# Performance work log

Hardware: AMD Instinct MI355X
Metric: run time of the kernel (lower is better)

Reference implementation:

```python
import jax, jax.numpy as jnp
import numpy as np

N, E, B, D, H, L = 50000, 800000, 16, 64, 128, 2


def _lin(h, w, b):
    return h @ w + b


def _scatter_mean(v, idx, n):
    s = jax.ops.segment_sum(v, idx, num_segments=n)
    c = jax.ops.segment_sum(jnp.ones((v.shape[0],), v.dtype), idx, num_segments=n)
    return s / jnp.maximum(c, 1.0)[:, None]


def setup_inputs() -> dict:
    key = jax.random.key(0)
    ks = iter(jax.random.split(key, 40))

    def p(*shape):
        return jax.random.normal(next(ks), shape, dtype=jnp.float32) * 0.05

    inp = {
        "x": jax.random.normal(next(ks), (N, D), dtype=jnp.float32),
        "edge_attr": jax.random.normal(next(ks), (E, D), dtype=jnp.float32),
        "u": jax.random.normal(next(ks), (B, D), dtype=jnp.float32),
        "e_w1": p(L, 4 * D, H), "e_b1": p(L, H),
        "e_w2": p(L, H, H), "e_b2": p(L, H),
        "e_w3": p(L, H, D), "e_b3": p(L, D),
        "n1_w1": p(L, 2 * D, H), "n1_b1": p(L, H),
        "n1_w2": p(L, H, H), "n1_b2": p(L, H),
        "n2_w1": p(L, D + H + D, H), "n2_b1": p(L, H),
        "n2_w2": p(L, H, D), "n2_b2": p(L, D),
        "g_w1": p(L, 3 * D, H), "g_b1": p(L, H),
        "g_w2": p(L, H, D), "g_b2": p(L, D),
        "edge_index": jax.random.randint(next(ks), (2, E), 0, N, dtype=jnp.int32),
        "batch": jnp.sort(jax.random.randint(next(ks), (N,), 0, B, dtype=jnp.int32)),
    }
    return inp


def _forward(x, edge_attr, u, params, edge_index, batch):
    row, col = edge_index[0], edge_index[1]
    eb = batch[row]  # [E] graph id per edge
    x0, e0, u0 = x, edge_attr, u
    for l in range(L):
        (e_w1, e_b1, e_w2, e_b2, e_w3, e_b3,
         n1_w1, n1_b1, n1_w2, n1_b2,
         n2_w1, n2_b1, n2_w2, n2_b2,
         g_w1, g_b1, g_w2, g_b2) = [pm[l] for pm in params]
        # Edge model: [E, e+2n+u] -> MLP -> [E, D]
        h = jnp.concatenate([x[row], x[col], edge_attr, u[eb]], axis=1)
        h = jax.nn.relu(_lin(h, e_w1, e_b1))
        h = jax.nn.relu(_lin(h, e_w2, e_b2))
        edge_attr = _lin(h, e_w3, e_b3)
        # Node model: gather src node + edge, MLP1, scatter_mean onto dest, MLP2
        se = jnp.concatenate([x[row], edge_attr], axis=1)  # [E, 2D]
        se = _lin(jax.nn.relu(_lin(se, n1_w1, n1_b1)), n1_w2, n1_b2)
        agg = _scatter_mean(se, col, N)  # [N, H]
        xh = jnp.concatenate([x, agg, u[batch]], axis=1)
        x = _lin(jax.nn.relu(_lin(xh, n2_w1, n2_b1)), n2_w2, n2_b2)
        # Global model: per-graph means of updated nodes/edges
        e_agg = _scatter_mean(edge_attr, eb, B)
        n_agg = _scatter_mean(x, batch, B)
        uh = jnp.concatenate([u, n_agg, e_agg], axis=1)
        u = _lin(jax.nn.relu(_lin(uh, g_w1, g_b1)), g_w2, g_b2)
    return x + x0, edge_attr + e0, u + u0


def reference(x, edge_attr, u, e_w1, e_b1, e_w2, e_b2, e_w3, e_b3, n1_w1, n1_b1, n1_w2, n1_b2, n2_w1, n2_b1, n2_w2, n2_b2, g_w1, g_b1, g_w2, g_b2, edge_index, batch):
    params = (e_w1, e_b1, e_w2, e_b2, e_w3, e_b3,
              n1_w1, n1_b1, n1_w2, n1_b2,
              n2_w1, n2_b1, n2_w2, n2_b2,
              g_w1, g_b1, g_w2, g_b2)
    return _forward(x, edge_attr, u, params, edge_index, batch)
```

## Files before the change

### kernel.cpp

```cpp
#include <hip/hip_runtime.h>

#define N_NODES 50000
#define E_EDGES 800000
#define NG 16
#define DD 64
#define HH 128
#define NB_SCAN 49

typedef __attribute__((ext_vector_type(8))) __bf16 bf16x8;
typedef __attribute__((ext_vector_type(4))) float f32x4;
typedef unsigned int uint;
typedef unsigned short ushort;
typedef __attribute__((ext_vector_type(4))) uint uint4v;

#define MFMA16(a,b,c) __builtin_amdgcn_mfma_f32_16x16x32_bf16((a),(b),(c),0,0,0)

__device__ __forceinline__ ushort f2bf(float f){
  uint u = __builtin_bit_cast(uint, f);
  u += 0x7fffu + ((u >> 16) & 1u);
  return (ushort)(u >> 16);
}
__device__ __forceinline__ uint pk2(float a, float b){
  return (uint)f2bf(a) | ((uint)f2bf(b) << 16);
}
__device__ __forceinline__ float bflo(uint u){ return __builtin_bit_cast(float, u << 16); }
__device__ __forceinline__ float bfhi(uint u){ return __builtin_bit_cast(float, u & 0xffff0000u); }

__device__ __forceinline__ bf16x8 ldfrag(const char* base, int row, int byteoff){
  uint4v v = *(const uint4v*)(base + row*256 + (byteoff ^ ((row & 7) << 4)));
  return __builtin_bit_cast(bf16x8, v);
}
__device__ __forceinline__ uint4v ld_chunk(const char* base, int row, int c16){
  return *(const uint4v*)(base + row*256 + ((c16*16) ^ ((row & 7) << 4)));
}
__device__ __forceinline__ void st_h(char* base, int row, int col, float v){
  *(ushort*)(base + row*256 + ((col*2) ^ ((row & 7) << 4))) = f2bf(v);
}
__device__ __forceinline__ void st_chunk(char* base, int row, int c16, uint4v v){
  *(uint4v*)(base + row*256 + ((c16*16) ^ ((row & 7) << 4))) = v;
}
__device__ __forceinline__ void pack16(char* dst, int r, int c16, const float* src){
  float4 lo = *(const float4*)src;
  float4 hi = *(const float4*)(src + 4);
  uint4v v; v.x = pk2(lo.x, lo.y); v.y = pk2(lo.z, lo.w);
  v.z = pk2(hi.x, hi.y); v.w = pk2(hi.z, hi.w);
  st_chunk(dst, r, c16, v);
}

__device__ __forceinline__ void stage_b(char* sB, const ushort* wt,
                                        int Nout, int Ktot, int koff, int t, int stride){
  for (int task = t; task < Nout*16; task += stride){
    int n = task >> 4, c = task & 15;
    uint4v v = *(const uint4v*)(wt + (long)n*Ktot + koff + c*8);
    st_chunk(sB, n, c, v);
  }
}

__device__ __forceinline__ void gemmN4(const char* A, const char* B,
                                       int mw, int nh, int l15, int lhi, f32x4* acc){
  #pragma unroll
  for (int kt = 0; kt < 4; ++kt){
    bf16x8 a = ldfrag(A, mw*16 + l15, kt*64 + lhi*16);
    #pragma unroll
    for (int n = 0; n < 4; ++n){
      bf16x8 bb = ldfrag(B, (nh*4 + n)*16 + l15, kt*64 + lhi*16);
      acc[n] = MFMA16(a, bb, acc[n]);
    }
  }
}
template<bool RELU>
__device__ __forceinline__ void epiN4(char* dst, const f32x4* acc, const float* bias,
                                      int mw, int nh, int l15, int lhi){
  #pragma unroll
  for (int n = 0; n < 4; ++n){
    int col = nh*64 + n*16 + l15;
    float bv = bias[col];
    #pragma unroll
    for (int j = 0; j < 4; ++j){
      int r = mw*16 + lhi*4 + j;
      float v = acc[n][j] + bv;
      if (RELU) v = fmaxf(v, 0.f);
      st_h(dst, r, col, v);
    }
  }
}

template<int NT>
__device__ __forceinline__ void gemm_acc(const char* A, const char* B,
                                         int wv, int l15, int lhi, f32x4* acc){
  #pragma unroll
  for (int kt = 0; kt < 4; ++kt){
    bf16x8 a = ldfrag(A, wv*16 + l15, kt*64 + lhi*16);
    #pragma unroll
    for (int n = 0; n < NT; ++n){
      bf16x8 bb = ldfrag(B, n*16 + l15, kt*64 + lhi*16);
      acc[n] = MFMA16(a, bb, acc[n]);
    }
  }
}
template<int NT, bool RELU>
__device__ __forceinline__ void epi_lds(char* dst, const f32x4* acc, const float* bias,
                                        int wv, int l15, int lhi){
  #pragma unroll
  for (int n = 0; n < NT; ++n){
    float bv = bias[n*16 + l15];
    #pragma unroll
    for (int j = 0; j < 4; ++j){
      int r = wv*16 + lhi*4 + j;
      float v = acc[n][j] + bv;
      if (RELU) v = fmaxf(v, 0.f);
      st_h(dst, r, n*16 + l15, v);
    }
  }
}

__global__ void pack_weights(const float* __restrict__ e1, const float* __restrict__ e2,
                             const float* __restrict__ e3, const float* __restrict__ n11,
                             const float* __restrict__ n12, const float* __restrict__ n21,
                             const float* __restrict__ n22, ushort* __restrict__ out){
  int idx = blockIdx.x * 256 + threadIdx.x;
  int l = idx / 131072, r = idx % 131072;
  const float* src; int K, N, off;
  if      (r <  32768){ src = e1;  K = 256; N = 128; off = 0; }
  else if (r <  49152){ src = e2;  K = 128; N = 128; off = 32768; }
  else if (r <  57344){ src = e3;  K = 128; N = 64;  off = 49152; }
  else if (r <  73728){ src = n11; K = 128; N = 128; off = 57344; }
  else if (r <  90112){ src = n12; K = 128; N = 128; off = 73728; }
  else if (r < 122880){ src = n21; K = 256; N = 128; off = 90112; }
  else                { src = n22; K = 128; N = 64;  off = 122880; }
  int q = r - off; int k = q / N; int n = q % N;
  out[(long)l*131072 + off + n*K + k] = f2bf(src[(long)l*K*N + q]);
}

__global__ void hist_kernel(const int* __restrict__ edge_index, const int* __restrict__ batch,
                            int* __restrict__ deg, float* __restrict__ cnt_eb){
  __shared__ float h[NG];
  int t = threadIdx.x;
  if (t < NG) h[t] = 0.f;
  __syncthreads();
  int e = blockIdx.x * 256 + t;
  if (e < E_EDGES){
    atomicAdd(deg + edge_index[E_EDGES + e], 1);
    atomicAdd(&h[batch[edge_index[e]]], 1.f);
  }
  __syncthreads();
  if (t < NG) atomicAdd(cnt_eb + t, h[t]);
}
__global__ void count_nodes_kernel(const int* __restrict__ batch, float* __restrict__ cnt_b){
  __shared__ float h[NG];
  int t = threadIdx.x;
  if (t < NG) h[t] = 0.f;
  __syncthreads();
  int n = blockIdx.x * 256 + t;
  if (n < N_NODES) atomicAdd(&h[batch[n]], 1.f);
  __syncthreads();
  if (t < NG) atomicAdd(cnt_b + t, h[t]);
}
__global__ void scan_a(const int* __restrict__ deg, int* __restrict__ bsum){
  __shared__ int red[1024];
  int i = blockIdx.x*1024 + threadIdx.x;
  red[threadIdx.x] = (i < N_NODES) ? deg[i] : 0;
  __syncthreads();
  for (int s = 512; s > 0; s >>= 1){
    if ((int)threadIdx.x < s) red[threadIdx.x] += red[threadIdx.x + s];
    __syncthreads();
  }
  if (threadIdx.x == 0) bsum[blockIdx.x] = red[0];
}
__global__ void scan_b(const int* __restrict__ bsum, int* __restrict__ bbase){
  if (threadIdx.x == 0){
    int run = 0;
    for (int b = 0; b < NB_SCAN; ++b){ int v = bsum[b]; bbase[b] = run; run += v; }
  }
}
__global__ void scan_c(const int* __restrict__ deg, const int* __restrict__ bbase,
                       int* __restrict__ off, int* __restrict__ cursor){
  __shared__ int sc[1024];
  int i = blockIdx.x*1024 + threadIdx.x;
  int v = (i < N_NODES) ? deg[i] : 0;
  sc[threadIdx.x] = v;
  __syncthreads();
  for (int d = 1; d < 1024; d <<= 1){
    int add = ((int)threadIdx.x >= d) ? sc[threadIdx.x - d] : 0;
    __syncthreads();
    sc[threadIdx.x] += add;
    __syncthreads();
  }
  if (i < N_NODES){
    int ex = sc[threadIdx.x] - v + bbase[blockIdx.x];
    off[i] = ex; cursor[i] = ex;
  }
}
__global__ void fill_kernel(const int* __restrict__ edge_index, int* __restrict__ cursor,
                            int* __restrict__ pos){
  int e = blockIdx.x*256 + threadIdx.x;
  if (e < E_EDGES){
    int c = edge_index[E_EDGES + e];
    pos[e] = atomicAdd(&cursor[c], 1);
  }
}

template<bool CSR>
__global__ __launch_bounds__(512, 4) void edge_kernel(
    const float* __restrict__ x_cur, const float* __restrict__ e_cur,
    const float* __restrict__ u_cur, const float* __restrict__ e_resid,
    const int* __restrict__ edge_index, const int* __restrict__ batch,
    const int* __restrict__ pos_arr,
    const ushort* __restrict__ w_e1, const ushort* __restrict__ w_e2,
    const ushort* __restrict__ w_e3, const ushort* __restrict__ w_n11,
    const ushort* __restrict__ w_n12,
    const float* __restrict__ b_e1, const float* __restrict__ b_e2,
    const float* __restrict__ b_e3, const float* __restrict__ b_n11,
    const float* __restrict__ b_n12,
    float* __restrict__ e_out, ushort* __restrict__ se_buf,
    float* __restrict__ agg_sum, float* __restrict__ e_agg, int has_resid)
{
  __shared__ __align__(16) char sA[16384];
  __shared__ __align__(16) char sB[32768];
  __shared__ __align__(16) char sH[16384];
  __shared__ int sRow[64], sCol[64], sEb[64];
  __shared__ float sEagg[NG*DD];

  const int t = threadIdx.x;
  const int wv = t >> 6, ln = t & 63, l15 = ln & 15, lhi = ln >> 4;
  const int mw = wv & 3, nh = wv >> 2;
  const int ebase = blockIdx.x * 64;

  if (t < 64){
    int r = edge_index[ebase + t];
    sRow[t] = r; sCol[t] = edge_index[E_EDGES + ebase + t]; sEb[t] = batch[r];
  }
  for (int i = t; i < NG*DD; i += 512) sEagg[i] = 0.f;
  __syncthreads();

  f32x4 acc1[4];
  #pragma unroll
  for (int n = 0; n < 4; ++n) acc1[n] = f32x4{0.f,0.f,0.f,0.f};
  for (int kh = 0; kh < 2; ++kh){
    for (int task = t; task < 1024; task += 512){
      int r = task >> 4, c = task & 15;
      const float* src;
      if (kh == 0) src = (c < 8) ? (x_cur + (long)sRow[r]*DD + c*8)
                                 : (x_cur + (long)sCol[r]*DD + (c-8)*8);
      else         src = (c < 8) ? (e_cur + (long)(ebase + r)*DD + c*8)
                                 : (u_cur + (long)sEb[r]*DD + (c-8)*8);
      pack16(sA, r, c, src);
    }
    stage_b(sB, w_e1, 128, 256, kh*128, t, 512);
    __syncthreads();
    gemmN4(sA, sB, mw, nh, l15, lhi, acc1);
    __syncthreads();
  }
  epiN4<true>(sH, acc1, b_e1, mw, nh, l15, lhi);
  stage_b(sB, w_e2, 128, 128, 0, t, 512);
  __syncthreads();

  f32x4 acc2[4];
  #pragma unroll
  for (int n = 0; n < 4; ++n) acc2[n] = f32x4{0.f,0.f,0.f,0.f};
  gemmN4(sH, sB, mw, nh, l15, lhi, acc2);
  __syncthreads();
  epiN4<true>(sA, acc2, b_e2, mw, nh, l15, lhi);
  stage_b(sB, w_e3, 64, 128, 0, t, 512);
  __syncthreads();

  f32x4 acc3[2];
  acc3[0] = f32x4{0.f,0.f,0.f,0.f}; acc3[1] = f32x4{0.f,0.f,0.f,0.f};
  #pragma unroll
  for (int kt = 0; kt < 4; ++kt){
    bf16x8 a = ldfrag(sA, mw*16 + l15, kt*64 + lhi*16);
    #pragma unroll
    for (int n = 0; n < 2; ++n){
      bf16x8 bb = ldfrag(sB, (nh*2 + n)*16 + l15, kt*64 + lhi*16);
      acc3[n] = MFMA16(a, bb, acc3[n]);
    }
  }
  float enew[2][4];
  #pragma unroll
  for (int n = 0; n < 2; ++n){
    int col = nh*32 + n*16 + l15;
    float bv = b_e3[col];
    #pragma unroll
    for (int j = 0; j < 4; ++j){
      int r = mw*16 + lhi*4 + j;
      float v = acc3[n][j] + bv;
      enew[n][j] = v;
      long eg = (long)(ebase + r)*DD + col;
      e_out[eg] = has_resid ? (v + e_resid[eg]) : v;
      atomicAdd(&sEagg[sEb[r]*DD + col], v);
    }
  }
  __syncthreads();

  #pragma unroll
  for (int n = 0; n < 2; ++n){
    #pragma unroll
    for (int j = 0; j < 4; ++j){
      int r = mw*16 + lhi*4 + j;
      st_h(sA, r, 64 + nh*32 + n*16 + l15, enew[n][j]);
    }
  }
  { int r = t >> 3, c = t & 7;
    pack16(sA, r, c, x_cur + (long)sRow[r]*DD + c*8); }
  stage_b(sB, w_n11, 128, 128, 0, t, 512);
  __syncthreads();

  f32x4 acc4[4];
  #pragma unroll
  for (int n = 0; n < 4; ++n) acc4[n] = f32x4{0.f,0.f,0.f,0.f};
  gemmN4(sA, sB, mw, nh, l15, lhi, acc4);
  __syncthreads();
  epiN4<true>(sH, acc4, b_n11, mw, nh, l15, lhi);
  stage_b(sB, w_n12, 128, 128, 0, t, 512);
  __syncthreads();

  f32x4 acc5[4];
  #pragma unroll
  for (int n = 0; n < 4; ++n) acc5[n] = f32x4{0.f,0.f,0.f,0.f};
  gemmN4(sH, sB, mw, nh, l15, lhi, acc5);

  if (CSR){
    epiN4<false>(sA, acc5, b_n12, mw, nh, l15, lhi);
    __syncthreads();
    int r = t >> 3, oct = t & 7;
    long p = pos_arr[ebase + r];
    uint4v v0 = ld_chunk(sA, r, oct*2);
    uint4v v1 = ld_chunk(sA, r, oct*2 + 1);
    *(uint4v*)(se_buf + p*128 + oct*16) = v0;
    *(uint4v*)(se_buf + p*128 + oct*16 + 8) = v1;
  } else {
    #pragma unroll
    for (int n = 0; n < 4; ++n){
      int col = nh*64 + n*16 + l15;
      float bv = b_n12[col];
      #pragma unroll
      for (int j = 0; j < 4; ++j){
        int r = mw*16 + lhi*4 + j;
        atomicAdd(agg_sum + (long)sCol[r]*HH + col, acc5[n][j] + bv);
      }
    }
  }
  for (int i = t; i < NG*DD; i += 512) atomicAdd(e_agg + i, sEagg[i]);
}

template<bool CSR>
__global__ __launch_bounds__(256, 2) void node_kernel(
    const float* __restrict__ x_cur, const float* __restrict__ u_cur,
    const float* __restrict__ x_resid, const int* __restrict__ batch,
    const ushort* __restrict__ se_buf, const int* __restrict__ deg,
    const int* __restrict__ off, const float* __restrict__ agg_sum,
    const ushort* __restrict__ w_n21, const ushort* __restrict__ w_n22,
    const float* __restrict__ b_n21, const float* __restrict__ b_n22,
    float* __restrict__ x_out, float* __restrict__ n_agg, int has_resid)
{
  __shared__ __align__(16) char sA[16384];
  __shared__ __align__(16) char sB[32768];
  __shared__ __align__(16) char sH[16384];
  __shared__ int sBat[64], sDeg[64], sOff[64];
  __shared__ float sRinv[64];
  __shared__ float sNagg[NG*DD];

  const int t = threadIdx.x;
  const int wv = t >> 6, ln = t & 63, l15 = ln & 15, lhi = ln >> 4;
  const int n0 = blockIdx.x * 64;

  if (t < 64){
    int nd = n0 + t;
    int ok = nd < N_NODES;
    sBat[t] = ok ? batch[nd] : 0;
    int d = ok ? deg[nd] : 0;
    sDeg[t] = d;
    sOff[t] = ok ? off[nd] : 0;
    sRinv[t] = 1.f / fmaxf((float)d, 1.f);
  }
  for (int i = t; i < NG*DD; i += 256) sNagg[i] = 0.f;
  __syncthreads();

  float s[32];
  const int r4 = t >> 2, q = t & 3;
  if (CSR){
    #pragma unroll
    for (int k = 0; k < 32; ++k) s[k] = 0.f;
    int d = sDeg[r4], o = sOff[r4];
    for (int i = 0; i < d; ++i){
      const ushort* src = se_buf + (long)(o + i)*HH + q*32;
      #pragma unroll
      for (int c = 0; c < 4; ++c){
        uint4v v = *(const uint4v*)(src + c*8);
        #pragma unroll
        for (int jj = 0; jj < 4; ++jj){
          s[c*8 + jj*2]     += bflo(v[jj]);
          s[c*8 + jj*2 + 1] += bfhi(v[jj]);
        }
      }
    }
    float riv = sRinv[r4];
    #pragma unroll
    for (int k = 0; k < 32; ++k) s[k] *= riv;
  }

  f32x4 acc[8];
  #pragma unroll
  for (int n = 0; n < 8; ++n) acc[n] = f32x4{0.f,0.f,0.f,0.f};

  for (int half = 0; half < 2; ++half){
    if (CSR){
      for (int task = t; task < 512; task += 256){
        int r = task >> 3, c = task & 7;
        int nd = n0 + r;
        bool ok = nd < N_NODES;
        float4 lo = {0,0,0,0}, hi = {0,0,0,0};
        if (ok){
          const float* src = (half == 0) ? (x_cur + (long)nd*DD + c*8)
                                         : (u_cur + (long)sBat[r]*DD + c*8);
          lo = *(const float4*)src; hi = *(const float4*)(src + 4);
        }
        uint4v v; v.x = pk2(lo.x, lo.y); v.y = pk2(lo.z, lo.w);
        v.z = pk2(hi.x, hi.y); v.w = pk2(hi.z, hi.w);
        st_chunk(sA, r, (half == 0) ? c : (8 + c), v);
      }
      if ((half == 0 && q < 2) || (half == 1 && q >= 2)){
        int cbase = (half == 0) ? (8 + q*4) : ((q - 2)*4);
        #pragma unroll
        for (int cc = 0; cc < 4; ++cc){
          uint4v v;
          v.x = pk2(s[cc*8+0], s[cc*8+1]); v.y = pk2(s[cc*8+2], s[cc*8+3]);
          v.z = pk2(s[cc*8+4], s[cc*8+5]); v.w = pk2(s[cc*8+6], s[cc*8+7]);
          st_chunk(sA, r4, cbase + cc, v);
        }
      }
    } else {
      for (int task = t; task < 1024; task += 256){
        int r = task >> 4, c = task & 15;
        int nd = n0 + r;
        bool ok = nd < N_NODES;
        float scale = 1.f;
        const float* src;
        if (half == 0){
          if (c < 8) src = x_cur + (long)nd*DD + c*8;
          else { src = agg_sum + (long)nd*HH + (c-8)*8; scale = sRinv[r]; }
        } else {
          if (c < 8){ src = agg_sum + (long)nd*HH + 64 + c*8; scale = sRinv[r]; }
          else src = u_cur + (long)sBat[r]*DD + (c-8)*8;
        }
        float4 lo = {0,0,0,0}, hi = {0,0,0,0};
        if (ok){ lo = *(const float4*)src; hi = *(const float4*)(src + 4); }
        uint4v v; v.x = pk2(lo.x*scale, lo.y*scale); v.y = pk2(lo.z*scale, lo.w*scale);
        v.z = pk2(hi.x*scale, hi.y*scale); v.w = pk2(hi.z*scale, hi.w*scale);
        st_chunk(sA, r, c, v);
      }
    }
    stage_b(sB, w_n21, 128, 256, half*128, t, 256);
    __syncthreads();
    gemm_acc<8>(sA, sB, wv, l15, lhi, acc);
    __syncthreads();
  }
  epi_lds<8, true>(sH, acc, b_n21, wv, l15, lhi);
  stage_b(sB, w_n22, 64, 128, 0, t, 256);
  __syncthreads();

  f32x4 acc2[4];
  #pragma unroll
  for (int n = 0; n < 4; ++n) acc2[n] = f32x4{0.f,0.f,0.f,0.f};
  gemm_acc<4>(sH, sB, wv, l15, lhi, acc2);

  #pragma unroll
  for (int n = 0; n < 4; ++n){
    float bv = b_n22[n*16 + l15];
    #pragma unroll
    for (int j = 0; j < 4; ++j){
      int r = wv*16 + lhi*4 + j;
      int nd = n0 + r;
      if (nd < N_NODES){
        int col = n*16 + l15;
        float v = acc2[n][j] + bv;
        long xg = (long)nd*DD + col;
        x_out[xg] = has_resid ? (v + x_resid[xg]) : v;
        atomicAdd(&sNagg[sBat[r]*DD + col], v);
      }
    }
  }
  __syncthreads();
  for (int i = t; i < NG*DD; i += 256) atomicAdd(n_agg + i, sNagg[i]);
}

__global__ void global_kernel(const float* __restrict__ u_cur, const float* __restrict__ n_agg,
                              const float* __restrict__ e_agg, const float* __restrict__ cnt_b,
                              const float* __restrict__ cnt_e,
                              const float* __restrict__ g_w1, const float* __restrict__ g_b1,
                              const float* __restrict__ g_w2, const float* __restrict__ g_b2,
                              const float* __restrict__ u_resid, float* __restrict__ u_out,
                              int has_resid)
{
  int g = blockIdx.x, t = threadIdx.x;
  __shared__ float uh[192];
  __shared__ float hb[128];
  float v;
  if (t < 64)       v = u_cur[g*64 + t];
  else if (t < 128) v = n_agg[g*64 + (t-64)] / fmaxf(cnt_b[g], 1.f);
  else              v = e_agg[g*64 + (t-128)] / fmaxf(cnt_e[g], 1.f);
  uh[t] = v;
  __syncthreads();
  if (t < 128){
    float s = g_b1[t];
    for (int k = 0; k < 192; ++k) s += uh[k] * g_w1[k*128 + t];
    hb[t] = fmaxf(s, 0.f);
  }
  __syncthreads();
  if (t < 64){
    float s = g_b2[t];
    for (int k = 0; k < 128; ++k) s += hb[k] * g_w2[k*64 + t];
    if (has_resid) s += u_resid[g*64 + t];
    u_out[g*64 + t] = s;
  }
}

extern "C" void kernel_launch(void* const* d_in, const int* in_sizes, int n_in,
                              void* d_out, int out_size, void* d_ws, size_t ws_size,
                              hipStream_t stream)
{
  const float* x0   = (const float*)d_in[0];
  const float* e0   = (const float*)d_in[1];
  const float* u0   = (const float*)d_in[2];
  const float* e_w1 = (const float*)d_in[3];
  const float* e_b1 = (const float*)d_in[4];
  const float* e_w2 = (const float*)d_in[5];
  const float* e_b2 = (const float*)d_in[6];
  const float* e_w3 = (const float*)d_in[7];
  const float* e_b3 = (const float*)d_in[8];
  const float* n1_w1 = (const float*)d_in[9];
  const float* n1_b1 = (const float*)d_in[10];
  const float* n1_w2 = (const float*)d_in[11];
  const float* n1_b2 = (const float*)d_in[12];
  const float* n2_w1 = (const float*)d_in[13];
  const float* n2_b1 = (const float*)d_in[14];
  const float* n2_w2 = (const float*)d_in[15];
  const float* n2_b2 = (const float*)d_in[16];
  const float* g_w1 = (const float*)d_in[17];
  const float* g_b1 = (const float*)d_in[18];
  const float* g_w2 = (const float*)d_in[19];
  const float* g_b2 = (const float*)d_in[20];
  const int* edge_index = (const int*)d_in[21];
  const int* batch      = (const int*)d_in[22];

  float* out_x = (float*)d_out;
  float* out_e = out_x + (long)N_NODES*DD;
  float* out_u = out_e + (long)E_EDGES*DD;

  char* ws = (char*)d_ws;
  int*   deg    = (int*)(ws + 0);
  int*   off    = (int*)(ws + 200000);
  int*   cursor = (int*)(ws + 400000);
  int*   bsum   = (int*)(ws + 600000);
  int*   bbase  = (int*)(ws + 600256);
  float* cnt_eb = (float*)(ws + 600512);
  float* cnt_b  = (float*)(ws + 600576);
  float* e_agg  = (float*)(ws + 600640);
  float* n_agg  = (float*)(ws + 604736);
  ushort* packed = (ushort*)(ws + 608832);
  const size_t big = 1133120;
  bool use_csr = ws_size >= (size_t)(big + 204800000 + 3200000);
  ushort* se_buf = (ushort*)(ws + big);
  int*    pos    = (int*)(ws + big + 204800000);
  float*  agg_sum = (float*)(ws + big);

  (void)hipMemsetAsync(deg, 0, 200000, stream);
  (void)hipMemsetAsync(cnt_eb, 0, 128, stream);
  pack_weights<<<1024, 256, 0, stream>>>(e_w1, e_w2, e_w3, n1_w1, n1_w2, n2_w1, n2_w2, packed);
  hist_kernel<<<3125, 256, 0, stream>>>(edge_index, batch, deg, cnt_eb);
  count_nodes_kernel<<<196, 256, 0, stream>>>(batch, cnt_b);
  if (use_csr){
    scan_a<<<NB_SCAN, 1024, 0, stream>>>(deg, bsum);
    scan_b<<<1, 64, 0, stream>>>(bsum, bbase);
    scan_c<<<NB_SCAN, 1024, 0, stream>>>(deg, bbase, off, cursor);
    fill_kernel<<<3125, 256, 0, stream>>>(edge_index, cursor, pos);
  }

  const float* xc = x0;
  const float* ec = e0;
  const float* uc = u0;
  for (int l = 0; l < 2; ++l){
    (void)hipMemsetAsync(e_agg, 0, 8192, stream);
    if (!use_csr)
      (void)hipMemsetAsync(agg_sum, 0, (size_t)N_NODES*HH*4, stream);
    const ushort* P = packed + (long)l*131072;
    if (use_csr){
      edge_kernel<true><<<E_EDGES/64, 512, 0, stream>>>(
          xc, ec, uc, e0, edge_index, batch, pos,
          P + 0, P + 32768, P + 49152, P + 57344, P + 73728,
          e_b1 + l*128, e_b2 + l*128, e_b3 + l*64, n1_b1 + l*128, n1_b2 + l*128,
          out_e, se_buf, agg_sum, e_agg, l == 1);
      node_kernel<true><<<782, 256, 0, stream>>>(
          xc, uc, x0, batch, se_buf, deg, off, agg_sum,
          P + 90112, P + 122880, n2_b1 + l*128, n2_b2 + l*64,
          out_x, n_agg, l == 1);
    } else {
      edge_kernel<false><<<E_EDGES/64, 512, 0, stream>>>(
          xc, ec, uc, e0, edge_index, batch, pos,
          P + 0, P + 32768, P + 49152, P + 57344, P + 73728,
          e_b1 + l*128, e_b2 + l*128, e_b3 + l*64, n1_b1 + l*128, n1_b2 + l*128,
          out_e, se_buf, agg_sum, e_agg, l == 1);
      node_kernel<false><<<782, 256, 0, stream>>>(
          xc, uc, x0, batch, se_buf, deg, off, agg_sum,
          P + 90112, P + 122880, n2_b1 + l*128, n2_b2 + l*64,
          out_x, n_agg, l == 1);
    }
    global_kernel<<<NG, 192, 0, stream>>>(
        uc, n_agg, e_agg, cnt_b, cnt_eb,
        g_w1 + l*192*128, g_b1 + l*128, g_w2 + l*128*64, g_b2 + l*64,
        u0, out_u, l == 1);
    xc = out_x; ec = out_e; uc = out_u;
  }
}
```

Baseline: 1.805 ms.

## Load edge-kernel weight fragments directly into registers and widen A tile to 512B rows

The edge kernel no longer stages weights into a shared sB buffer. Each wave loads its B fragments straight from global memory into registers. The A tile becomes 512-byte rows holding the full 256-wide concatenated input in one pass, so the x[row] slice can be reused for the node MLP without regathering it. This drops 32KB of LDS per block, which should raise occupancy, and removes several barriers and LDS round trips. In exchange it adds register pressure and repeated global or L2 weight reads per wave.

```diff
diff --git a/kernel.cpp b/kernel.cpp
--- a/kernel.cpp
+++ b/kernel.cpp
@@ -47,6 +47,91 @@
   st_chunk(dst, r, c16, v);
 }
 
+__device__ __forceinline__ bf16x8 ldfrag512(const char* base, int row, int byteoff){
+  uint4v v = *(const uint4v*)(base + row*512 + (byteoff ^ ((row & 7) << 4)));
+  return __builtin_bit_cast(bf16x8, v);
+}
+__device__ __forceinline__ uint4v ld_chunk512(const char* base, int row, int c16){
+  return *(const uint4v*)(base + row*512 + ((c16*16) ^ ((row & 7) << 4)));
+}
+__device__ __forceinline__ void st_h512(char* base, int row, int col, float v){
+  *(ushort*)(base + row*512 + ((col*2) ^ ((row & 7) << 4))) = f2bf(v);
+}
+__device__ __forceinline__ void pack16_512(char* dst, int r, int c16, const float* src){
+  float4 lo = *(const float4*)src;
+  float4 hi = *(const float4*)(src + 4);
+  uint4v v; v.x = pk2(lo.x, lo.y); v.y = pk2(lo.z, lo.w);
+  v.z = pk2(hi.x, hi.y); v.w = pk2(hi.z, hi.w);
+  *(uint4v*)(dst + r*512 + ((c16*16) ^ ((r & 7) << 4))) = v;
+}
+
+__device__ __forceinline__ void loadB16(bf16x8 (&b)[4][4], const ushort* wt, int K, int koff,
+                                        int nbase, int l15, int lhi){
+  #pragma unroll
+  for (int kt = 0; kt < 4; ++kt)
+    #pragma unroll
+    for (int n = 0; n < 4; ++n)
+      b[kt][n] = *(const bf16x8*)(wt + (long)((nbase + n)*16 + l15)*K + koff + kt*32 + lhi*8);
+}
+__device__ __forceinline__ void loadB8(bf16x8 (&b)[4][2], const ushort* wt, int K,
+                                       int nbase, int l15, int lhi){
+  #pragma unroll
+  for (int kt = 0; kt < 4; ++kt)
+    #pragma unroll
+    for (int n = 0; n < 2; ++n)
+      b[kt][n] = *(const bf16x8*)(wt + (long)((nbase + n)*16 + l15)*K + kt*32 + lhi*8);
+}
+__device__ __forceinline__ void gemmA512(const char* A, int abyte, bf16x8 (&b)[4][4],
+                                         int mw, int l15, int lhi, f32x4* acc){
+  #pragma unroll
+  for (int kt = 0; kt < 4; ++kt){
+    bf16x8 a = ldfrag512(A, mw*16 + l15, abyte + kt*64 + lhi*16);
+    #pragma unroll
+    for (int n = 0; n < 4; ++n) acc[n] = MFMA16(a, b[kt][n], acc[n]);
+  }
+}
+__device__ __forceinline__ void gemmA256(const char* A, bf16x8 (&b)[4][4],
+                                         int mw, int l15, int lhi, f32x4* acc){
+  #pragma unroll
+  for (int kt = 0; kt < 4; ++kt){
+    bf16x8 a = ldfrag(A, mw*16 + l15, kt*64 + lhi*16);
+    #pragma unroll
+    for (int n = 0; n < 4; ++n) acc[n] = MFMA16(a, b[kt][n], acc[n]);
+  }
+}
+template<bool RELU>
+__device__ __forceinline__ void epiN4(char* dst, const f32x4* acc, const float* bias,
+                                      int mw, int nh, int l15, int lhi){
+  #pragma unroll
+  for (int n = 0; n < 4; ++n){
+    int col = nh*64 + n*16 + l15;
+    float bv = bias[col];
+    #pragma unroll
+    for (int j = 0; j < 4; ++j){
+      int r = mw*16 + lhi*4 + j;
+      float v = acc[n][j] + bv;
+      if (RELU) v = fmaxf(v, 0.f);
+      st_h(dst, r, col, v);
+    }
+  }
+}
+template<bool RELU>
+__device__ __forceinline__ void epi512(char* dst, int colbase, const f32x4* acc, const float* bias,
+                                       int mw, int nh, int l15, int lhi){
+  #pragma unroll
+  for (int n = 0; n < 4; ++n){
+    int col = nh*64 + n*16 + l15;
+    float bv = bias[col];
+    #pragma unroll
+    for (int j = 0; j < 4; ++j){
+      int r = mw*16 + lhi*4 + j;
+      float v = acc[n][j] + bv;
+      if (RELU) v = fmaxf(v, 0.f);
+      st_h512(dst, r, colbase + col, v);
+    }
+  }
+}
+
 __device__ __forceinline__ void stage_b(char* sB, const ushort* wt,
                                         int Nout, int Ktot, int koff, int t, int stride){
   for (int task = t; task < Nout*16; task += stride){
@@ -55,36 +140,6 @@
     st_chunk(sB, n, c, v);
   }
 }
-
-__device__ __forceinline__ void gemmN4(const char* A, const char* B,
-                                       int mw, int nh, int l15, int lhi, f32x4* acc){
-  #pragma unroll
-  for (int kt = 0; kt < 4; ++kt){
-    bf16x8 a = ldfrag(A, mw*16 + l15, kt*64 + lhi*16);
-    #pragma unroll
-    for (int n = 0; n < 4; ++n){
-      bf16x8 bb = ldfrag(B, (nh*4 + n)*16 + l15, kt*64 + lhi*16);
-      acc[n] = MFMA16(a, bb, acc[n]);
-    }
-  }
-}
-template<bool RELU>
-__device__ __forceinline__ void epiN4(char* dst, const f32x4* acc, const float* bias,
-                                      int mw, int nh, int l15, int lhi){
-  #pragma unroll
-  for (int n = 0; n < 4; ++n){
-    int col = nh*64 + n*16 + l15;
-    float bv = bias[col];
-    #pragma unroll
-    for (int j = 0; j < 4; ++j){
-      int r = mw*16 + lhi*4 + j;
-      float v = acc[n][j] + bv;
-      if (RELU) v = fmaxf(v, 0.f);
-      st_h(dst, r, col, v);
-    }
-  }
-}
-
 template<int NT>
 __device__ __forceinline__ void gemm_acc(const char* A, const char* B,
                                          int wv, int l15, int lhi, f32x4* acc){
@@ -215,8 +270,7 @@
     float* __restrict__ e_out, ushort* __restrict__ se_buf,
     float* __restrict__ agg_sum, float* __restrict__ e_agg, int has_resid)
 {
-  __shared__ __align__(16) char sA[16384];
-  __shared__ __align__(16) char sB[32768];
+  __shared__ __align__(16) char sA[32768];
   __shared__ __align__(16) char sH[16384];
   __shared__ int sRow[64], sCol[64], sEb[64];
   __shared__ float sEagg[NG*DD];
@@ -233,49 +287,47 @@
   for (int i = t; i < NG*DD; i += 512) sEagg[i] = 0.f;
   __syncthreads();
 
-  f32x4 acc1[4];
-  #pragma unroll
-  for (int n = 0; n < 4; ++n) acc1[n] = f32x4{0.f,0.f,0.f,0.f};
-  for (int kh = 0; kh < 2; ++kh){
-    for (int task = t; task < 1024; task += 512){
-      int r = task >> 4, c = task & 15;
-      const float* src;
-      if (kh == 0) src = (c < 8) ? (x_cur + (long)sRow[r]*DD + c*8)
-                                 : (x_cur + (long)sCol[r]*DD + (c-8)*8);
-      else         src = (c < 8) ? (e_cur + (long)(ebase + r)*DD + c*8)
-                                 : (u_cur + (long)sEb[r]*DD + (c-8)*8);
-      pack16(sA, r, c, src);
-    }
-    stage_b(sB, w_e1, 128, 256, kh*128, t, 512);
-    __syncthreads();
-    gemmN4(sA, sB, mw, nh, l15, lhi, acc1);
-    __syncthreads();
-  }
-  epiN4<true>(sH, acc1, b_e1, mw, nh, l15, lhi);
-  stage_b(sB, w_e2, 128, 128, 0, t, 512);
-  __syncthreads();
-
-  f32x4 acc2[4];
-  #pragma unroll
-  for (int n = 0; n < 4; ++n) acc2[n] = f32x4{0.f,0.f,0.f,0.f};
-  gemmN4(sH, sB, mw, nh, l15, lhi, acc2);
-  __syncthreads();
-  epiN4<true>(sA, acc2, b_e2, mw, nh, l15, lhi);
-  stage_b(sB, w_e3, 64, 128, 0, t, 512);
+  #pragma unroll
+  for (int it = 0; it < 4; ++it){
+    int task = t + it*512;
+    int r = task >> 5, c = task & 31;
+    const float* src;
+    if      (c <  8) src = x_cur + (long)sRow[r]*DD + c*8;
+    else if (c < 16) src = x_cur + (long)sCol[r]*DD + (c-8)*8;
+    else if (c < 24) src = e_cur + (long)(ebase + r)*DD + (c-16)*8;
+    else             src = u_cur + (long)sEb[r]*DD + (c-24)*8;
+    pack16_512(sA, r, c, src);
+  }
+  bf16x8 b[4][4];
+  loadB16(b, w_e1, 256, 0, nh*4, l15, lhi);
+  __syncthreads();
+
+  f32x4 acc[4];
+  #pragma unroll
+  for (int n = 0; n < 4; ++n) acc[n] = f32x4{0.f,0.f,0.f,0.f};
+  gemmA512(sA, 0, b, mw, l15, lhi, acc);
+  loadB16(b, w_e1, 256, 128, nh*4, l15, lhi);
+  gemmA512(sA, 256, b, mw, l15, lhi, acc);
+  epiN4<true>(sH, acc, b_e1, mw, nh, l15, lhi);
+  loadB16(b, w_e2, 128, 0, nh*4, l15, lhi);
+  __syncthreads();
+
+  #pragma unroll
+  for (int n = 0; n < 4; ++n) acc[n] = f32x4{0.f,0.f,0.f,0.f};
+  gemmA256(sH, b, mw, l15, lhi, acc);
+  epi512<true>(sA, 128, acc, b_e2, mw, nh, l15, lhi);
+  bf16x8 b3[4][2];
+  loadB8(b3, w_e3, 128, nh*2, l15, lhi);
   __syncthreads();
 
   f32x4 acc3[2];
   acc3[0] = f32x4{0.f,0.f,0.f,0.f}; acc3[1] = f32x4{0.f,0.f,0.f,0.f};
   #pragma unroll
   for (int kt = 0; kt < 4; ++kt){
-    bf16x8 a = ldfrag(sA, mw*16 + l15, kt*64 + lhi*16);
-    #pragma unroll
-    for (int n = 0; n < 2; ++n){
-      bf16x8 bb = ldfrag(sB, (nh*2 + n)*16 + l15, kt*64 + lhi*16);
-      acc3[n] = MFMA16(a, bb, acc3[n]);
-    }
-  }
-  float enew[2][4];
+    bf16x8 a = ldfrag512(sA, mw*16 + l15, 256 + kt*64 + lhi*16);
+    #pragma unroll
+    for (int n = 0; n < 2; ++n) acc3[n] = MFMA16(a, b3[kt][n], acc3[n]);
+  }
   #pragma unroll
   for (int n = 0; n < 2; ++n){
     int col = nh*32 + n*16 + l15;
@@ -284,48 +336,33 @@
     for (int j = 0; j < 4; ++j){
       int r = mw*16 + lhi*4 + j;
       float v = acc3[n][j] + bv;
-      enew[n][j] = v;
       long eg = (long)(ebase + r)*DD + col;
       e_out[eg] = has_resid ? (v + e_resid[eg]) : v;
       atomicAdd(&sEagg[sEb[r]*DD + col], v);
-    }
-  }
-  __syncthreads();
-
-  #pragma unroll
-  for (int n = 0; n < 2; ++n){
-    #pragma unroll
-    for (int j = 0; j < 4; ++j){
-      int r = mw*16 + lhi*4 + j;
-      st_h(sA, r, 64 + nh*32 + n*16 + l15, enew[n][j]);
-    }
-  }
-  { int r = t >> 3, c = t & 7;
-    pack16(sA, r, c, x_cur + (long)sRow[r]*DD + c*8); }
-  stage_b(sB, w_n11, 128, 128, 0, t, 512);
-  __syncthreads();
-
-  f32x4 acc4[4];
-  #pragma unroll
-  for (int n = 0; n < 4; ++n) acc4[n] = f32x4{0.f,0.f,0.f,0.f};
-  gemmN4(sA, sB, mw, nh, l15, lhi, acc4);
-  __syncthreads();
-  epiN4<true>(sH, acc4, b_n11, mw, nh, l15, lhi);
-  stage_b(sB, w_n12, 128, 128, 0, t, 512);
-  __syncthreads();
-
-  f32x4 acc5[4];
-  #pragma unroll
-  for (int n = 0; n < 4; ++n) acc5[n] = f32x4{0.f,0.f,0.f,0.f};
-  gemmN4(sH, sB, mw, nh, l15, lhi, acc5);
+      st_h512(sA, r, 64 + col, v);
+    }
+  }
+  loadB16(b, w_n11, 128, 0, nh*4, l15, lhi);
+  __syncthreads();
+
+  #pragma unroll
+  for (int n = 0; n < 4; ++n) acc[n] = f32x4{0.f,0.f,0.f,0.f};
+  gemmA512(sA, 0, b, mw, l15, lhi, acc);
+  epiN4<true>(sH, acc, b_n11, mw, nh, l15, lhi);
+  loadB16(b, w_n12, 128, 0, nh*4, l15, lhi);
+  __syncthreads();
+
+  #pragma unroll
+  for (int n = 0; n < 4; ++n) acc[n] = f32x4{0.f,0.f,0.f,0.f};
+  gemmA256(sH, b, mw, l15, lhi, acc);
 
   if (CSR){
-    epiN4<false>(sA, acc5, b_n12, mw, nh, l15, lhi);
+    epi512<false>(sA, 0, acc, b_n12, mw, nh, l15, lhi);
     __syncthreads();
     int r = t >> 3, oct = t & 7;
     long p = pos_arr[ebase + r];
-    uint4v v0 = ld_chunk(sA, r, oct*2);
-    uint4v v1 = ld_chunk(sA, r, oct*2 + 1);
+    uint4v v0 = ld_chunk512(sA, r, oct*2);
+    uint4v v1 = ld_chunk512(sA, r, oct*2 + 1);
     *(uint4v*)(se_buf + p*128 + oct*16) = v0;
     *(uint4v*)(se_buf + p*128 + oct*16 + 8) = v1;
   } else {
@@ -336,9 +373,10 @@
       #pragma unroll
       for (int j = 0; j < 4; ++j){
         int r = mw*16 + lhi*4 + j;
-        atomicAdd(agg_sum + (long)sCol[r]*HH + col, acc5[n][j] + bv);
+        atomicAdd(agg_sum + (long)sCol[r]*HH + col, acc[n][j] + bv);
       }
     }
+    __syncthreads();
   }
   for (int i = t; i < NG*DD; i += 512) atomicAdd(e_agg + i, sEagg[i]);
 }
```

Result: slower. 2.861 ms (+58.5%).

## Make edge kernel persistent with software-pipelined gathers and weight staging

Applied to the files above, without the earlier changes.

Turns the edge kernel into a persistent kernel with 512 blocks looping over 64-edge tiles. While the current tile computes, it prefetches the next tile's indices, gathered node/edge features and the next weight slab into registers. The warp tiling becomes 2x2 MFMA tiles per wave, the e3 weights live in registers, and the per-block e_agg flush happens once per block rather than once per tile. The aim is to hide global gather and weight-staging latency and cut launch and reduction overhead, at the cost of more registers (launch bounds lowered from 4 to 2 blocks) and a lot of manual barrier choreography.

```diff
diff --git a/kernel.cpp b/kernel.cpp
--- a/kernel.cpp
+++ b/kernel.cpp
@@ -6,6 +6,7 @@
 #define DD 64
 #define HH 128
 #define NB_SCAN 49
+#define NTILES 12500
 
 typedef __attribute__((ext_vector_type(8))) __bf16 bf16x8;
 typedef __attribute__((ext_vector_type(4))) float f32x4;
@@ -25,6 +26,11 @@
 }
 __device__ __forceinline__ float bflo(uint u){ return __builtin_bit_cast(float, u << 16); }
 __device__ __forceinline__ float bfhi(uint u){ return __builtin_bit_cast(float, u & 0xffff0000u); }
+
+__device__ __forceinline__ void lds_barrier(){
+  asm volatile("s_waitcnt lgkmcnt(0)" ::: "memory");
+  __builtin_amdgcn_s_barrier();
+}
 
 __device__ __forceinline__ bf16x8 ldfrag(const char* base, int row, int byteoff){
   uint4v v = *(const uint4v*)(base + row*256 + (byteoff ^ ((row & 7) << 4)));
@@ -55,36 +61,6 @@
     st_chunk(sB, n, c, v);
   }
 }
-
-__device__ __forceinline__ void gemmN4(const char* A, const char* B,
-                                       int mw, int nh, int l15, int lhi, f32x4* acc){
-  #pragma unroll
-  for (int kt = 0; kt < 4; ++kt){
-    bf16x8 a = ldfrag(A, mw*16 + l15, kt*64 + lhi*16);
-    #pragma unroll
-    for (int n = 0; n < 4; ++n){
-      bf16x8 bb = ldfrag(B, (nh*4 + n)*16 + l15, kt*64 + lhi*16);
-      acc[n] = MFMA16(a, bb, acc[n]);
-    }
-  }
-}
-template<bool RELU>
-__device__ __forceinline__ void epiN4(char* dst, const f32x4* acc, const float* bias,
-                                      int mw, int nh, int l15, int lhi){
-  #pragma unroll
-  for (int n = 0; n < 4; ++n){
-    int col = nh*64 + n*16 + l15;
-    float bv = bias[col];
-    #pragma unroll
-    for (int j = 0; j < 4; ++j){
-      int r = mw*16 + lhi*4 + j;
-      float v = acc[n][j] + bv;
-      if (RELU) v = fmaxf(v, 0.f);
-      st_h(dst, r, col, v);
-    }
-  }
-}
-
 template<int NT>
 __device__ __forceinline__ void gemm_acc(const char* A, const char* B,
                                          int wv, int l15, int lhi, f32x4* acc){
@@ -201,7 +177,7 @@
 }
 
 template<bool CSR>
-__global__ __launch_bounds__(512, 4) void edge_kernel(
+__global__ __launch_bounds__(512, 2) void edge_kernel(
     const float* __restrict__ x_cur, const float* __restrict__ e_cur,
     const float* __restrict__ u_cur, const float* __restrict__ e_resid,
     const int* __restrict__ edge_index, const int* __restrict__ batch,
@@ -216,130 +192,232 @@
     float* __restrict__ agg_sum, float* __restrict__ e_agg, int has_resid)
 {
   __shared__ __align__(16) char sA[16384];
+  __shared__ __align__(16) char sH[16384];
   __shared__ __align__(16) char sB[32768];
-  __shared__ __align__(16) char sH[16384];
-  __shared__ int sRow[64], sCol[64], sEb[64];
   __shared__ float sEagg[NG*DD];
+  __shared__ int sRow[2][64], sCol[2][64], sEb[2][64];
 
   const int t = threadIdx.x;
   const int wv = t >> 6, ln = t & 63, l15 = ln & 15, lhi = ln >> 4;
-  const int mw = wv & 3, nh = wv >> 2;
-  const int ebase = blockIdx.x * 64;
-
+  const int mw = wv & 1, ng = wv >> 1;
+  const int cc = t & 31, rr = t >> 5;
+
+  bf16x8 b3[4];
+  #pragma unroll
+  for (int kt = 0; kt < 4; ++kt)
+    b3[kt] = *(const bf16x8*)(w_e3 + (long)(ng*16 + l15)*128 + kt*32 + lhi*8);
+
+  for (int i = t; i < NG*DD; i += 512) sEagg[i] = 0.f;
+
+  uint4v wA[4];
+  float4 raw[8];
+  uint4v gk[4];
+
+  auto LOADW = [&](const ushort* W, int K, int KOFF){
+    #pragma unroll
+    for (int it = 0; it < 4; ++it)
+      wA[it] = *(const uint4v*)(W + (long)(it*32 + (t >> 4))*K + KOFF + (t & 15)*8);
+  };
+  auto STOREW = [&](){
+    #pragma unroll
+    for (int it = 0; it < 4; ++it)
+      st_chunk(sB, it*32 + (t >> 4), t & 15, wA[it]);
+  };
+  auto GATHER = [&](int base, int p, bool doU, bool doRest){
+    #pragma unroll
+    for (int it = 0; it < 4; ++it){
+      int r = it*16 + rr;
+      const float* s;
+      bool go;
+      if (cc < 8)      { s = x_cur + (long)sRow[p][r]*DD + cc*8;          go = doRest; }
+      else if (cc < 16){ s = x_cur + (long)sCol[p][r]*DD + (cc-8)*8;      go = doRest; }
+      else if (cc < 24){ s = e_cur + (long)(base + r)*DD + (cc-16)*8;     go = doRest; }
+      else             { s = u_cur + (long)sEb[p][r]*DD + (cc-24)*8;      go = doU;   }
+      if (go){ raw[2*it] = *(const float4*)s; raw[2*it+1] = *(const float4*)(s + 4); }
+    }
+  };
+  auto PACK = [&](){
+    #pragma unroll
+    for (int it = 0; it < 4; ++it){
+      uint4v v;
+      v.x = pk2(raw[2*it].x, raw[2*it].y);   v.y = pk2(raw[2*it].z, raw[2*it].w);
+      v.z = pk2(raw[2*it+1].x, raw[2*it+1].y); v.w = pk2(raw[2*it+1].z, raw[2*it+1].w);
+      gk[it] = v;
+    }
+  };
+  f32x4 acc[2][2];
+  auto ZACC = [&](){
+    #pragma unroll
+    for (int m = 0; m < 2; ++m){ acc[m][0] = f32x4{0,0,0,0}; acc[m][1] = f32x4{0,0,0,0}; }
+  };
+  auto GEMMP = [&](const char* base){
+    #pragma unroll
+    for (int kt = 0; kt < 4; ++kt){
+      bf16x8 a0 = ldfrag(base, mw*32 + l15,      kt*64 + lhi*16);
+      bf16x8 a1 = ldfrag(base, mw*32 + 16 + l15, kt*64 + lhi*16);
+      bf16x8 bb0 = ldfrag(sB, (ng*2    )*16 + l15, kt*64 + lhi*16);
+      bf16x8 bb1 = ldfrag(sB, (ng*2 + 1)*16 + l15, kt*64 + lhi*16);
+      acc[0][0] = MFMA16(a0, bb0, acc[0][0]);
+      acc[0][1] = MFMA16(a0, bb1, acc[0][1]);
+      acc[1][0] = MFMA16(a1, bb0, acc[1][0]);
+      acc[1][1] = MFMA16(a1, bb1, acc[1][1]);
+    }
+  };
+  auto EPI = [&](char* dst, const float* bias, bool relu){
+    #pragma unroll
+    for (int m = 0; m < 2; ++m)
+      #pragma unroll
+      for (int n = 0; n < 2; ++n){
+        int col = ng*32 + n*16 + l15;
+        float bv = bias[col];
+        #pragma unroll
+        for (int j = 0; j < 4; ++j){
+          float v = acc[m][n][j] + bv;
+          if (relu) v = fmaxf(v, 0.f);
+          st_h(dst, mw*32 + m*16 + lhi*4 + j, col, v);
+        }
+      }
+  };
+
+  int tile = blockIdx.x;
+  int par = 0;
   if (t < 64){
-    int r = edge_index[ebase + t];
-    sRow[t] = r; sCol[t] = edge_index[E_EDGES + ebase + t]; sEb[t] = batch[r];
-  }
-  for (int i = t; i < NG*DD; i += 512) sEagg[i] = 0.f;
-  __syncthreads();
-
-  f32x4 acc1[4];
-  #pragma unroll
-  for (int n = 0; n < 4; ++n) acc1[n] = f32x4{0.f,0.f,0.f,0.f};
-  for (int kh = 0; kh < 2; ++kh){
-    for (int task = t; task < 1024; task += 512){
-      int r = task >> 4, c = task & 15;
-      const float* src;
-      if (kh == 0) src = (c < 8) ? (x_cur + (long)sRow[r]*DD + c*8)
-                                 : (x_cur + (long)sCol[r]*DD + (c-8)*8);
-      else         src = (c < 8) ? (e_cur + (long)(ebase + r)*DD + c*8)
-                                 : (u_cur + (long)sEb[r]*DD + (c-8)*8);
-      pack16(sA, r, c, src);
-    }
-    stage_b(sB, w_e1, 128, 256, kh*128, t, 512);
-    __syncthreads();
-    gemmN4(sA, sB, mw, nh, l15, lhi, acc1);
-    __syncthreads();
-  }
-  epiN4<true>(sH, acc1, b_e1, mw, nh, l15, lhi);
-  stage_b(sB, w_e2, 128, 128, 0, t, 512);
-  __syncthreads();
-
-  f32x4 acc2[4];
-  #pragma unroll
-  for (int n = 0; n < 4; ++n) acc2[n] = f32x4{0.f,0.f,0.f,0.f};
-  gemmN4(sH, sB, mw, nh, l15, lhi, acc2);
-  __syncthreads();
-  epiN4<true>(sA, acc2, b_e2, mw, nh, l15, lhi);
-  stage_b(sB, w_e3, 64, 128, 0, t, 512);
-  __syncthreads();
-
-  f32x4 acc3[2];
-  acc3[0] = f32x4{0.f,0.f,0.f,0.f}; acc3[1] = f32x4{0.f,0.f,0.f,0.f};
-  #pragma unroll
-  for (int kt = 0; kt < 4; ++kt){
-    bf16x8 a = ldfrag(sA, mw*16 + l15, kt*64 + lhi*16);
-    #pragma unroll
-    for (int n = 0; n < 2; ++n){
-      bf16x8 bb = ldfrag(sB, (nh*2 + n)*16 + l15, kt*64 + lhi*16);
-      acc3[n] = MFMA16(a, bb, acc3[n]);
-    }
-  }
-  float enew[2][4];
-  #pragma unroll
-  for (int n = 0; n < 2; ++n){
-    int col = nh*32 + n*16 + l15;
-    float bv = b_e3[col];
-    #pragma unroll
-    for (int j = 0; j < 4; ++j){
-      int r = mw*16 + lhi*4 + j;
-      float v = acc3[n][j] + bv;
-      enew[n][j] = v;
-      long eg = (long)(ebase + r)*DD + col;
-      e_out[eg] = has_resid ? (v + e_resid[eg]) : v;
-      atomicAdd(&sEagg[sEb[r]*DD + col], v);
-    }
-  }
-  __syncthreads();
-
-  #pragma unroll
-  for (int n = 0; n < 2; ++n){
-    #pragma unroll
-    for (int j = 0; j < 4; ++j){
-      int r = mw*16 + lhi*4 + j;
-      st_h(sA, r, 64 + nh*32 + n*16 + l15, enew[n][j]);
-    }
-  }
-  { int r = t >> 3, c = t & 7;
-    pack16(sA, r, c, x_cur + (long)sRow[r]*DD + c*8); }
-  stage_b(sB, w_n11, 128, 128, 0, t, 512);
-  __syncthreads();
-
-  f32x4 acc4[4];
-  #pragma unroll
-  for (int n = 0; n < 4; ++n) acc4[n] = f32x4{0.f,0.f,0.f,0.f};
-  gemmN4(sA, sB, mw, nh, l15, lhi, acc4);
-  __syncthreads();
-  epiN4<true>(sH, acc4, b_n11, mw, nh, l15, lhi);
-  stage_b(sB, w_n12, 128, 128, 0, t, 512);
-  __syncthreads();
-
-  f32x4 acc5[4];
-  #pragma unroll
-  for (int n = 0; n < 4; ++n) acc5[n] = f32x4{0.f,0.f,0.f,0.f};
-  gemmN4(sH, sB, mw, nh, l15, lhi, acc5);
-
-  if (CSR){
-    epiN4<false>(sA, acc5, b_n12, mw, nh, l15, lhi);
-    __syncthreads();
-    int r = t >> 3, oct = t & 7;
-    long p = pos_arr[ebase + r];
-    uint4v v0 = ld_chunk(sA, r, oct*2);
-    uint4v v1 = ld_chunk(sA, r, oct*2 + 1);
-    *(uint4v*)(se_buf + p*128 + oct*16) = v0;
-    *(uint4v*)(se_buf + p*128 + oct*16 + 8) = v1;
-  } else {
-    #pragma unroll
-    for (int n = 0; n < 4; ++n){
-      int col = nh*64 + n*16 + l15;
-      float bv = b_n12[col];
+    int r0 = edge_index[tile*64 + t];
+    sRow[0][t] = r0; sCol[0][t] = edge_index[E_EDGES + tile*64 + t];
+    sEb[0][t] = batch[r0];
+  }
+  LOADW(w_e1, 256, 0);
+  __syncthreads();
+  GATHER(tile*64, 0, true, true);
+  STOREW();
+  PACK();
+  lds_barrier();
+
+  for (; tile < NTILES; tile += gridDim.x){
+    const int ebase = tile*64;
+    const int nt = tile + gridDim.x;
+    const bool hn = nt < NTILES;
+    const int q = par ^ 1;
+
+    if (cc < 16){
       #pragma unroll
-      for (int j = 0; j < 4; ++j){
-        int r = mw*16 + lhi*4 + j;
-        atomicAdd(agg_sum + (long)sCol[r]*HH + col, acc5[n][j] + bv);
-      }
-    }
-  }
+      for (int it = 0; it < 4; ++it) st_chunk(sA, it*16 + rr, cc, gk[it]);
+    }
+    LOADW(w_e1, 256, 128);
+    lds_barrier();
+
+    ZACC();
+    GEMMP(sA);
+    int iR = 0, iC = 0;
+    if (hn && t < 64){
+      iR = edge_index[nt*64 + t];
+      iC = edge_index[E_EDGES + nt*64 + t];
+    }
+    lds_barrier();
+
+    if (cc >= 16){
+      #pragma unroll
+      for (int it = 0; it < 4; ++it) st_chunk(sA, it*16 + rr, cc - 16, gk[it]);
+    }
+    STOREW();
+    lds_barrier();
+
+    GEMMP(sA);
+    EPI(sH, b_e1, true);
+    LOADW(w_e2, 128, 0);
+    int iB = 0;
+    if (hn && t < 64){
+      sRow[q][t] = iR; sCol[q][t] = iC;
+      iB = batch[iR];
+    }
+    lds_barrier();
+
+    STOREW();
+    lds_barrier();
+
+    ZACC();
+    GEMMP(sH);
+    EPI(sA, b_e2, true);
+    LOADW(w_n11, 128, 0);
+    if (hn && t < 64) sEb[q][t] = iB;
+    lds_barrier();
+
+    {
+      f32x4 a3[2];
+      a3[0] = f32x4{0,0,0,0}; a3[1] = f32x4{0,0,0,0};
+      #pragma unroll
+      for (int kt = 0; kt < 4; ++kt){
+        bf16x8 a0 = ldfrag(sA, mw*32 + l15,      kt*64 + lhi*16);
+        bf16x8 a1 = ldfrag(sA, mw*32 + 16 + l15, kt*64 + lhi*16);
+        a3[0] = MFMA16(a0, b3[kt], a3[0]);
+        a3[1] = MFMA16(a1, b3[kt], a3[1]);
+      }
+      int col = ng*16 + l15;
+      float bv = b_e3[col];
+      #pragma unroll
+      for (int m = 0; m < 2; ++m)
+        #pragma unroll
+        for (int j = 0; j < 4; ++j){
+          int r = mw*32 + m*16 + lhi*4 + j;
+          float v = a3[m][j] + bv;
+          long eg = (long)(ebase + r)*DD + col;
+          e_out[eg] = has_resid ? (v + e_resid[eg]) : v;
+          atomicAdd(&sEagg[sEb[par][r]*DD + col], v);
+          st_h(sH, r, 64 + col, v);
+        }
+      if (cc < 8){
+        #pragma unroll
+        for (int it = 0; it < 4; ++it) st_chunk(sH, it*16 + rr, cc, gk[it]);
+      }
+      STOREW();
+    }
+    lds_barrier();
+
+    ZACC();
+    GEMMP(sH);
+    EPI(sA, b_n11, true);
+    LOADW(w_n12, 128, 0);
+    if (hn) GATHER(nt*64, q, false, true);
+    lds_barrier();
+
+    STOREW();
+    if (hn) GATHER(nt*64, q, true, false);
+    lds_barrier();
+
+    ZACC();
+    GEMMP(sA);
+    if (CSR){
+      EPI(sH, b_n12, false);
+    } else {
+      #pragma unroll
+      for (int m = 0; m < 2; ++m)
+        #pragma unroll
+        for (int n = 0; n < 2; ++n){
+          int col = ng*32 + n*16 + l15;
+          float bv = b_n12[col];
+          #pragma unroll
+          for (int j = 0; j < 4; ++j)
+            atomicAdd(agg_sum + (long)sCol[par][mw*32 + m*16 + lhi*4 + j]*HH + col,
+                      acc[m][n][j] + bv);
+        }
+    }
+    if (hn) LOADW(w_e1, 256, 0);
+    lds_barrier();
+
+    if (CSR){
+      int r = t >> 3, oct = t & 7;
+      long p = pos_arr[ebase + r];
+      uint4v v0 = ld_chunk(sH, r, oct*2);
+      uint4v v1 = ld_chunk(sH, r, oct*2 + 1);
+      *(uint4v*)(se_buf + p*128 + oct*16) = v0;
+      *(uint4v*)(se_buf + p*128 + oct*16 + 8) = v1;
+    }
+    if (hn){ STOREW(); PACK(); }
+    par = q;
+    lds_barrier();
+  }
+
+  __syncthreads();
   for (int i = t; i < NG*DD; i += 512) atomicAdd(e_agg + i, sEagg[i]);
 }
 
@@ -422,11 +500,11 @@
       if ((half == 0 && q < 2) || (half == 1 && q >= 2)){
         int cbase = (half == 0) ? (8 + q*4) : ((q - 2)*4);
         #pragma unroll
-        for (int cc = 0; cc < 4; ++cc){
+        for (int ccv = 0; ccv < 4; ++ccv){
           uint4v v;
-          v.x = pk2(s[cc*8+0], s[cc*8+1]); v.y = pk2(s[cc*8+2], s[cc*8+3]);
-          v.z = pk2(s[cc*8+4], s[cc*8+5]); v.w = pk2(s[cc*8+6], s[cc*8+7]);
-          st_chunk(sA, r4, cbase + cc, v);
+          v.x = pk2(s[ccv*8+0], s[ccv*8+1]); v.y = pk2(s[ccv*8+2], s[ccv*8+3]);
+          v.z = pk2(s[ccv*8+4], s[ccv*8+5]); v.w = pk2(s[ccv*8+6], s[ccv*8+7]);
+          st_chunk(sA, r4, cbase + ccv, v);
         }
       }
     } else {
@@ -585,7 +663,7 @@
       (void)hipMemsetAsync(agg_sum, 0, (size_t)N_NODES*HH*4, stream);
     const ushort* P = packed + (long)l*131072;
     if (use_csr){
-      edge_kernel<true><<<E_EDGES/64, 512, 0, stream>>>(
+      edge_kernel<true><<<512, 512, 0, stream>>>(
           xc, ec, uc, e0, edge_index, batch, pos,
           P + 0, P + 32768, P + 49152, P + 57344, P + 73728,
           e_b1 + l*128, e_b2 + l*128, e_b3 + l*64, n1_b1 + l*128, n1_b2 + l*128,
@@ -595,7 +673,7 @@
           P + 90112, P + 122880, n2_b1 + l*128, n2_b2 + l*64,
           out_x, n_agg, l == 1);
     } else {
-      edge_kernel<false><<<E_EDGES/64, 512, 0, stream>>>(
+      edge_kernel<false><<<512, 512, 0, stream>>>(
           xc, ec, uc, e0, edge_index, batch, pos,
           P + 0, P + 32768, P + 49152, P + 57344, P + 73728,
           e_b1 + l*128, e_b2 + l*128, e_b3 + l*64, n1_b1 + l*128, n1_b2 + l*128,
```

Result: slower. 2.219 ms (+23.0%).
